# Kernel optimization log

Hardware: AMD Instinct MI355X
Metric: run time of the kernel (lower is better)

Reference implementation:

```python
import jax, jax.numpy as jnp
import numpy as np

GRID = (32, 512, 512)  # volumetric query grid

def _fade(t):
    # quintic fade: 6t^5 - 15t^4 + 10t^3
    return t * t * t * (t * (t * 6.0 - 15.0) + 10.0)

def _lerp(a, b, t):
    return a + t * (b - a)

def _hash(perm, *indices):
    # chained permutation-table lookup: r = perm[(r + idx) % 256]
    r = jnp.zeros_like(indices[0])
    for idx in indices:
        r = perm[(r + idx) % 256]
    return r

def setup_inputs() -> dict:
    key = jax.random.key(0)
    kx, ky, kz = jax.random.split(key, 3)
    # coordinates uniform in [0, 64) so many lattice cells are covered
    x = jax.random.uniform(kx, GRID, dtype=jnp.float32) * 64.0
    y = jax.random.uniform(ky, GRID, dtype=jnp.float32) * 64.0
    z = jax.random.uniform(kz, GRID, dtype=jnp.float32) * 64.0
    rng = np.random.default_rng(0)
    perm = jnp.asarray(rng.permutation(256), dtype=jnp.int32)
    grad3 = jnp.asarray([
        [1, 1, 0], [-1, 1, 0], [1, -1, 0], [-1, -1, 0],
        [1, 0, 1], [-1, 0, 1], [1, 0, -1], [-1, 0, -1],
        [0, 1, 1], [0, -1, 1], [0, 1, -1], [0, -1, -1]], dtype=jnp.float32)
    return {"x": x, "y": y, "z": z, "perm": perm, "grad3": grad3}

def reference(x, y, z, perm, grad3):
    fx, fy, fz = jnp.floor(x), jnp.floor(y), jnp.floor(z)
    xi = fx.astype(jnp.int32) & 255
    yi = fy.astype(jnp.int32) & 255
    zi = fz.astype(jnp.int32) & 255
    xf, yf, zf = x - fx, y - fy, z - fz
    u, v, w = _fade(xf), _fade(yf), _fade(zf)

    aaa = _hash(perm, xi, yi, zi) % 12
    aab = _hash(perm, xi, yi, zi + 1) % 12
    aba = _hash(perm, xi, yi + 1, zi) % 12
    abb = _hash(perm, xi, yi + 1, zi + 1) % 12
    baa = _hash(perm, xi + 1, yi, zi) % 12
    bab = _hash(perm, xi + 1, yi, zi + 1) % 12
    bba = _hash(perm, xi + 1, yi + 1, zi) % 12
    bbb = _hash(perm, xi + 1, yi + 1, zi + 1) % 12

    def dot3(gi, dx, dy, dz):
        g = grad3[gi]  # gather [..., 3]
        return g[..., 0] * dx + g[..., 1] * dy + g[..., 2] * dz

    g_aaa = dot3(aaa, xf, yf, zf)
    g_aab = dot3(aab, xf, yf, zf - 1)
    g_aba = dot3(aba, xf, yf - 1, zf)
    g_abb = dot3(abb, xf, yf - 1, zf - 1)
    g_baa = dot3(baa, xf - 1, yf, zf)
    g_bab = dot3(bab, xf - 1, yf, zf - 1)
    g_bba = dot3(bba, xf - 1, yf - 1, zf)
    g_bbb = dot3(bbb, xf - 1, yf - 1, zf - 1)

    x1 = _lerp(g_aaa, g_baa, u)
    x2 = _lerp(g_aba, g_bba, u)
    x3 = _lerp(g_aab, g_bab, u)
    x4 = _lerp(g_abb, g_bbb, u)
    y1 = _lerp(x1, x2, v)
    y2 = _lerp(x3, x4, v)
    return _lerp(y1, y2, w)
```

## Files before the change

kernel.cpp:

```cpp
#include <hip/hip_runtime.h>

#define TPB 256
#define NBLOCKS 2048

__device__ __forceinline__ float fade_f(float t) {
    return t * t * t * (t * (t * 6.0f - 15.0f) + 10.0f);
}

__device__ __forceinline__ float lerp_f(float a, float b, float t) {
    return fmaf(t, b - a, a);
}

__device__ __forceinline__ float gdot(unsigned gi, float dx, float dy, float dz) {
    unsigned g = gi >> 2;
    float c1 = (g < 2u) ? dx : dy;
    float c2 = (g == 0u) ? dy : dz;
    unsigned u1 = __float_as_uint(c1) ^ ((gi & 1u) << 31);
    unsigned u2 = __float_as_uint(c2) ^ ((gi & 2u) << 30);
    return __uint_as_float(u1) + __uint_as_float(u2);
}

__global__ __launch_bounds__(TPB, 4) void perlin_kernel(
    const float* __restrict__ xg, const float* __restrict__ yg,
    const float* __restrict__ zg, const int* __restrict__ perm,
    float* __restrict__ out, int nquads)
{
    __shared__ unsigned T[256 * 32];

    for (int s = threadIdx.x; s < 256 * 32; s += TPB) {
        unsigned pv = (unsigned)perm[s >> 5];
        T[s] = pv | ((pv % 12u) << 8);
    }
    __syncthreads();

    const unsigned* Tl = T + (threadIdx.x & 31);

    const float4* x4 = (const float4*)xg;
    const float4* y4 = (const float4*)yg;
    const float4* z4 = (const float4*)zg;
    float4* o4 = (float4*)out;

    const int stride = gridDim.x * TPB;
    for (int q = blockIdx.x * TPB + threadIdx.x; q < nquads; q += stride) {
        float4 xv = x4[q], yv = y4[q], zv = z4[q];
        float xa[4] = {xv.x, xv.y, xv.z, xv.w};
        float ya[4] = {yv.x, yv.y, yv.z, yv.w};
        float za[4] = {zv.x, zv.y, zv.z, zv.w};
        float res[4];

        #pragma unroll
        for (int e = 0; e < 4; ++e) {
            float X = xa[e], Y = ya[e], Z = za[e];
            float fx = floorf(X), fy = floorf(Y), fz = floorf(Z);
            float xf = X - fx, yf = Y - fy, zf = Z - fz;
            int xi = ((int)fx) & 255;
            int yi = ((int)fy) & 255;
            int zi = ((int)fz) & 255;
            float u = fade_f(xf), v = fade_f(yf), w = fade_f(zf);
            float xf1 = xf - 1.0f, yf1 = yf - 1.0f, zf1 = zf - 1.0f;

            #define LK(i) Tl[((unsigned)(i) & 255u) << 5]
            unsigned A  = LK(xi),         B  = LK(xi + 1);
            unsigned aa = LK(A + yi),     ab = LK(A + yi + 1);
            unsigned ba = LK(B + yi),     bb = LK(B + yi + 1);
            unsigned haaa = LK(aa + zi) >> 8, haab = LK(aa + zi + 1) >> 8;
            unsigned haba = LK(ab + zi) >> 8, habb = LK(ab + zi + 1) >> 8;
            unsigned hbaa = LK(ba + zi) >> 8, hbab = LK(ba + zi + 1) >> 8;
            unsigned hbba = LK(bb + zi) >> 8, hbbb = LK(bb + zi + 1) >> 8;
            #undef LK

            float g_aaa = gdot(haaa, xf,  yf,  zf);
            float g_aab = gdot(haab, xf,  yf,  zf1);
            float g_aba = gdot(haba, xf,  yf1, zf);
            float g_abb = gdot(habb, xf,  yf1, zf1);
            float g_baa = gdot(hbaa, xf1, yf,  zf);
            float g_bab = gdot(hbab, xf1, yf,  zf1);
            float g_bba = gdot(hbba, xf1, yf1, zf);
            float g_bbb = gdot(hbbb, xf1, yf1, zf1);

            float l1 = lerp_f(g_aaa, g_baa, u);
            float l2 = lerp_f(g_aba, g_bba, u);
            float l3 = lerp_f(g_aab, g_bab, u);
            float l4 = lerp_f(g_abb, g_bbb, u);
            float m1 = lerp_f(l1, l2, v);
            float m2 = lerp_f(l3, l4, v);
            res[e] = lerp_f(m1, m2, w);
        }
        o4[q] = make_float4(res[0], res[1], res[2], res[3]);
    }
}

extern "C" void kernel_launch(void* const* d_in, const int* in_sizes, int n_in,
                              void* d_out, int out_size, void* d_ws, size_t ws_size,
                              hipStream_t stream) {
    const float* x   = (const float*)d_in[0];
    const float* y   = (const float*)d_in[1];
    const float* z   = (const float*)d_in[2];
    const int* perm  = (const int*)d_in[3];
    float* out = (float*)d_out;
    int nquads = out_size >> 2;
    perlin_kernel<<<NBLOCKS, TPB, 0, stream>>>(x, y, z, perm, out, nquads);
}
```

Before: 149.6 us.

## Pre-scale perm table entries to byte offsets and halve LDS replication

```diff
diff --git a/kernel.cpp b/kernel.cpp
--- a/kernel.cpp
+++ b/kernel.cpp
@@ -2,38 +2,40 @@
 
 #define TPB 256
 #define NBLOCKS 2048
+#define REPL 16
 
 __device__ __forceinline__ float fade_f(float t) {
-    return t * t * t * (t * (t * 6.0f - 15.0f) + 10.0f);
+    return t * t * t * fmaf(t, fmaf(t, 6.0f, -15.0f), 10.0f);
 }
 
 __device__ __forceinline__ float lerp_f(float a, float b, float t) {
     return fmaf(t, b - a, a);
 }
 
-__device__ __forceinline__ float gdot(unsigned gi, float dx, float dy, float dz) {
-    unsigned g = gi >> 2;
-    float c1 = (g < 2u) ? dx : dy;
-    float c2 = (g == 0u) ? dy : dz;
-    unsigned u1 = __float_as_uint(c1) ^ ((gi & 1u) << 31);
-    unsigned u2 = __float_as_uint(c2) ^ ((gi & 2u) << 30);
-    return __uint_as_float(u1) + __uint_as_float(u2);
+__device__ __forceinline__ float gdot_w(unsigned w, float dx, float dy, float dz) {
+    unsigned gi = w & 0x3Fu;
+    float c1 = (gi < 8u) ? dx : dy;
+    float c2 = (gi < 4u) ? dy : dz;
+    unsigned s1 = w << 31;
+    unsigned s2 = (w << 30) & 0x80000000u;
+    return __uint_as_float(__float_as_uint(c1) ^ s1)
+         + __uint_as_float(__float_as_uint(c2) ^ s2);
 }
 
-__global__ __launch_bounds__(TPB, 4) void perlin_kernel(
+__global__ __launch_bounds__(TPB, 8) void perlin_kernel(
     const float* __restrict__ xg, const float* __restrict__ yg,
     const float* __restrict__ zg, const int* __restrict__ perm,
     float* __restrict__ out, int nquads)
 {
-    __shared__ unsigned T[256 * 32];
+    __shared__ unsigned T[256 * REPL];
 
-    for (int s = threadIdx.x; s < 256 * 32; s += TPB) {
-        unsigned pv = (unsigned)perm[s >> 5];
-        T[s] = pv | ((pv % 12u) << 8);
+    for (int s = threadIdx.x; s < 256 * REPL; s += TPB) {
+        unsigned pv = (unsigned)perm[s >> 4];
+        T[s] = (pv << 6) | (pv % 12u);
     }
     __syncthreads();
 
-    const unsigned* Tl = T + (threadIdx.x & 31);
+    const char* Tl = (const char*)T + ((threadIdx.x & (REPL - 1)) << 2);
 
     const float4* x4 = (const float4*)xg;
     const float4* y4 = (const float4*)yg;
@@ -46,37 +48,38 @@
         float xa[4] = {xv.x, xv.y, xv.z, xv.w};
         float ya[4] = {yv.x, yv.y, yv.z, yv.w};
         float za[4] = {zv.x, zv.y, zv.z, zv.w};
-        float res[4];
+        float4 res;
+        float* rp = &res.x;
 
         #pragma unroll
         for (int e = 0; e < 4; ++e) {
             float X = xa[e], Y = ya[e], Z = za[e];
             float fx = floorf(X), fy = floorf(Y), fz = floorf(Z);
             float xf = X - fx, yf = Y - fy, zf = Z - fz;
-            int xi = ((int)fx) & 255;
-            int yi = ((int)fy) & 255;
-            int zi = ((int)fz) & 255;
+            unsigned x6 = ((unsigned)(int)fx << 6) & 0x3FC0u;
+            unsigned y6 = ((unsigned)(int)fy << 6);
+            unsigned z6 = ((unsigned)(int)fz << 6);
             float u = fade_f(xf), v = fade_f(yf), w = fade_f(zf);
             float xf1 = xf - 1.0f, yf1 = yf - 1.0f, zf1 = zf - 1.0f;
 
-            #define LK(i) Tl[((unsigned)(i) & 255u) << 5]
-            unsigned A  = LK(xi),         B  = LK(xi + 1);
-            unsigned aa = LK(A + yi),     ab = LK(A + yi + 1);
-            unsigned ba = LK(B + yi),     bb = LK(B + yi + 1);
-            unsigned haaa = LK(aa + zi) >> 8, haab = LK(aa + zi + 1) >> 8;
-            unsigned haba = LK(ab + zi) >> 8, habb = LK(ab + zi + 1) >> 8;
-            unsigned hbaa = LK(ba + zi) >> 8, hbab = LK(ba + zi + 1) >> 8;
-            unsigned hbba = LK(bb + zi) >> 8, hbbb = LK(bb + zi + 1) >> 8;
+            #define LK(off) (*(const unsigned*)(Tl + ((off) & 0x3FC0u)))
+            unsigned A  = LK(x6),          B  = LK(x6 + 64);
+            unsigned aa = LK(A + y6),      ab = LK(A + y6 + 64);
+            unsigned ba = LK(B + y6),      bb = LK(B + y6 + 64);
+            unsigned waaa = LK(aa + z6),   waab = LK(aa + z6 + 64);
+            unsigned waba = LK(ab + z6),   wabb = LK(ab + z6 + 64);
+            unsigned wbaa = LK(ba + z6),   wbab = LK(ba + z6 + 64);
+            unsigned wbba = LK(bb + z6),   wbbb = LK(bb + z6 + 64);
             #undef LK
 
-            float g_aaa = gdot(haaa, xf,  yf,  zf);
-            float g_aab = gdot(haab, xf,  yf,  zf1);
-            float g_aba = gdot(haba, xf,  yf1, zf);
-            float g_abb = gdot(habb, xf,  yf1, zf1);
-            float g_baa = gdot(hbaa, xf1, yf,  zf);
-            float g_bab = gdot(hbab, xf1, yf,  zf1);
-            float g_bba = gdot(hbba, xf1, yf1, zf);
-            float g_bbb = gdot(hbbb, xf1, yf1, zf1);
+            float g_aaa = gdot_w(waaa, xf,  yf,  zf);
+            float g_aab = gdot_w(waab, xf,  yf,  zf1);
+            float g_aba = gdot_w(waba, xf,  yf1, zf);
+            float g_abb = gdot_w(wabb, xf,  yf1, zf1);
+            float g_baa = gdot_w(wbaa, xf1, yf,  zf);
+            float g_bab = gdot_w(wbab, xf1, yf,  zf1);
+            float g_bba = gdot_w(wbba, xf1, yf1, zf);
+            float g_bbb = gdot_w(wbbb, xf1, yf1, zf1);
 
             float l1 = lerp_f(g_aaa, g_baa, u);
             float l2 = lerp_f(g_aba, g_bba, u);
@@ -84,9 +87,9 @@
             float l4 = lerp_f(g_abb, g_bbb, u);
             float m1 = lerp_f(l1, l2, v);
             float m2 = lerp_f(l3, l4, v);
-            res[e] = lerp_f(m1, m2, w);
+            rp[e] = lerp_f(m1, m2, w);
         }
-        o4[q] = make_float4(res[0], res[1], res[2], res[3]);
+        o4[q] = res;
     }
 }
 
```

Measured after the change: 141.6 us. 1.06x faster.
